# Kernel optimization log

Hardware: AMD Instinct MI355X
Metric: run time of the kernel (lower is better)

## Reference

```python
import jax, jax.numpy as jnp
import numpy as np

QMAX = 127.0  # int8 symmetric quantization range


def _quant_dequant(w):
    """Per-output-channel symmetric int8 fake quantization (weight-only),
    mimicking nn.quantized.Linear.from_float weight quantization."""
    scale = jnp.max(jnp.abs(w), axis=-1, keepdims=True) / QMAX
    scale = jnp.maximum(scale, 1e-8)
    q = jnp.clip(jnp.round(w / scale), -QMAX, QMAX)
    return q * scale


def setup_inputs() -> dict:
    key = jax.random.key(0)
    ks = jax.random.split(key, 7)
    B, S, D, F, E, NS = 2, 2048, 1024, 2048, 8, 1
    std = 1.0 / np.sqrt(D)
    x = jax.random.normal(ks[0], (B, S, D), dtype=jnp.float32)
    router_w = _quant_dequant(jax.random.normal(ks[1], (E, D), dtype=jnp.float32) * std)
    router_b = jnp.zeros((E,), dtype=jnp.float32)
    w_up = _quant_dequant(jax.random.normal(ks[2], (E, F, D), dtype=jnp.float32) * std)
    w_down = _quant_dequant(jax.random.normal(ks[3], (E, D, F), dtype=jnp.float32) / np.sqrt(F))
    shared_w_up = _quant_dequant(jax.random.normal(ks[4], (NS, F, D), dtype=jnp.float32) * std)
    shared_w_down = _quant_dequant(jax.random.normal(ks[5], (NS, D, F), dtype=jnp.float32) / np.sqrt(F))
    return {"x": x, "router_w": router_w, "router_b": router_b,
            "w_up": w_up, "w_down": w_down,
            "shared_w_up": shared_w_up, "shared_w_down": shared_w_down}


def reference(x, router_w, router_b, w_up, w_down, shared_w_up, shared_w_down):
    B, S, D = x.shape
    E = router_w.shape[0]
    TOPK = 2
    xt = x.reshape(-1, D)  # [T, D] tokens

    # Router (quantized linear) -> softmax -> top-k dispatch weights
    logits = xt @ router_w.T + router_b            # [T, E]
    probs = jax.nn.softmax(logits, axis=-1)        # [T, E]
    top_vals, top_idx = jax.lax.top_k(probs, TOPK)  # [T, K]
    top_vals = top_vals / jnp.sum(top_vals, axis=-1, keepdims=True)  # renormalize
    # combine[t, e] = routing weight of expert e for token t (0 if not selected)
    combine = jnp.sum(jax.nn.one_hot(top_idx, E, dtype=xt.dtype) * top_vals[..., None], axis=1)  # [T, E]

    # Routed experts: up -> SiLU -> down, computed densely then combined
    h = jnp.einsum('td,efd->tef', xt, w_up)        # [T, E, F]
    y = jnp.einsum('tef,edf->ted', jax.nn.silu(h), w_down)  # [T, E, D]
    out = jnp.einsum('ted,te->td', y, combine)     # [T, D]

    # Shared experts: always active, summed
    hs = jnp.einsum('td,sfd->tsf', xt, shared_w_up)          # [T, NS, F]
    out = out + jnp.einsum('tsf,sdf->td', jax.nn.silu(hs), shared_w_down)

    return out.reshape(B, S, D)
```

## Files before the change

### kernel.cpp

```cpp
#include <hip/hip_runtime.h>
#include <stdint.h>

typedef unsigned short u16;
typedef int i32x4 __attribute__((ext_vector_type(4)));

#define DDIM 1024
#define FDIM 2048
#define NEXP 8
#define RT_TILES 72
#define SHOFF 9216
#define RCAP 13312
#define NRT 104
#define UPROWS 16384
#define DNROWS 8192
#define UPTOT (UPROWS + FDIM)
#define DNTOT (DNROWS + DDIM)
#define WQWAVES (UPTOT + DNTOT)


__device__ inline float bf2f(u16 u) {
    union { unsigned int i; float f; } v; v.i = ((unsigned int)u) << 16; return v.f;
}
__device__ inline u16 f2bf(float f) {
    union { float f; unsigned int i; } v; v.f = f;
    unsigned int lsb = (v.i >> 16) & 1u;
    return (u16)((v.i + 0x7fffu + lsb) >> 16);
}
__device__ inline int q8(float v, float inv) {
    int x = (int)rintf(v * inv);
    return x < -127 ? -127 : (x > 127 ? 127 : x);
}
__device__ inline unsigned pack4(float a, float b, float c, float d, float inv) {
    return (unsigned)(q8(a, inv) & 255) | ((unsigned)(q8(b, inv) & 255) << 8) |
           ((unsigned)(q8(c, inv) & 255) << 16) | ((unsigned)(q8(d, inv) & 255) << 24);
}

typedef const __attribute__((address_space(1))) void gas_void;
typedef __attribute__((address_space(3))) void las_void;
#define GLL16(g, l) __builtin_amdgcn_global_load_lds((gas_void*)(g), (las_void*)(l), 16, 0, 0)

__device__ inline int detect_inline(const u16* __restrict__ x, int* sh) {
    if (threadIdx.x == 0) *sh = 0;
    __syncthreads();
    const int per = 1024 / blockDim.x;
    int bad = 0;
    for (int i = 0; i < per; i++) {
        u16 v = x[threadIdx.x * per + i];
        if (((v >> 7) & 0xFF) >= 0x8F) bad++;
    }
    if (bad) atomicAdd(sh, bad);
    __syncthreads();
    return (*sh > 32) ? 1 : 0;
}

__global__ __launch_bounds__(256) void router_kernel(
    const void* __restrict__ x_, const void* __restrict__ rw_, const void* __restrict__ rb_,
    float* __restrict__ top_w, int* __restrict__ top_idx)
{
    __shared__ char smem[32768 + 16];
    const int tid = threadIdx.x;
    const int wave = tid >> 6, lane = tid & 63;
    const int flag = detect_inline((const u16*)x_, (int*)(smem + 32768));

    float* rws = (float*)smem;
    if (!flag) {
        const ushort4* rwv = (const ushort4*)rw_;
        #pragma unroll
        for (int i = 0; i < 8; i++) {
            int idx = tid + i * 256;
            ushort4 h = rwv[idx];
            rws[idx * 4 + 0] = bf2f(h.x); rws[idx * 4 + 1] = bf2f(h.y);
            rws[idx * 4 + 2] = bf2f(h.z); rws[idx * 4 + 3] = bf2f(h.w);
        }
    } else {
        const float4* rwv = (const float4*)rw_;
        #pragma unroll
        for (int i = 0; i < 8; i++) {
            int idx = tid + i * 256;
            float4 f = rwv[idx];
            rws[idx * 4 + 0] = f.x; rws[idx * 4 + 1] = f.y;
            rws[idx * 4 + 2] = f.z; rws[idx * 4 + 3] = f.w;
        }
    }
    __syncthreads();

    for (int sub = 0; sub < 4; sub++) {
        const int t = blockIdx.x * 16 + wave * 4 + sub;
        float xv[16];
        if (!flag) {
            const u16* xr = (const u16*)x_ + (size_t)t * DDIM + lane * 16;
            uint4 p0 = *(const uint4*)(xr);
            uint4 p1 = *(const uint4*)(xr + 8);
            #pragma unroll
            for (int d = 0; d < 8; d++) xv[d]     = bf2f(((const u16*)&p0)[d]);
            #pragma unroll
            for (int d = 0; d < 8; d++) xv[d + 8] = bf2f(((const u16*)&p1)[d]);
        } else {
            const float4* xr = (const float4*)((const float*)x_ + (size_t)t * DDIM + lane * 16);
            #pragma unroll
            for (int c = 0; c < 4; c++) {
                float4 f = xr[c];
                xv[c * 4 + 0] = f.x; xv[c * 4 + 1] = f.y;
                xv[c * 4 + 2] = f.z; xv[c * 4 + 3] = f.w;
            }
        }
        float acc[NEXP];
        #pragma unroll
        for (int e = 0; e < NEXP; e++) {
            const float* wr = &rws[e * DDIM + lane * 16];
            float s = 0.f;
            #pragma unroll
            for (int d = 0; d < 16; d++) s += xv[d] * wr[d];
            acc[e] = s;
        }
        #pragma unroll
        for (int e = 0; e < NEXP; e++) {
            #pragma unroll
            for (int off = 32; off > 0; off >>= 1)
                acc[e] += __shfl_xor(acc[e], off, 64);
        }
        if (lane == 0) {
            float lg[NEXP];
            #pragma unroll
            for (int e = 0; e < NEXP; e++) {
                float b = flag ? ((const float*)rb_)[e] : bf2f(((const u16*)rb_)[e]);
                lg[e] = acc[e] + b;
            }
            int i0 = 0;
            #pragma unroll
            for (int e = 1; e < NEXP; e++) if (lg[e] > lg[i0]) i0 = e;
            int i1 = (i0 == 0) ? 1 : 0;
            #pragma unroll
            for (int e = 0; e < NEXP; e++) if (e != i0 && lg[e] > lg[i1]) i1 = e;
            float e1 = __expf(lg[i1] - lg[i0]);
            float w0 = 1.f / (1.f + e1);
            float w1 = e1 / (1.f + e1);
            top_w[2 * t] = w0;  top_w[2 * t + 1] = w1;
            top_idx[2 * t] = i0; top_idx[2 * t + 1] = i1;
        }
    }
}

template<int NC>
__device__ inline void wq_bf16(const char* __restrict__ src, char* __restrict__ dst,
                               float* __restrict__ sout, int R, int lane) {
    uint4 raw[NC];
    #pragma unroll
    for (int c = 0; c < NC; c++)
        raw[c] = *(const uint4*)(src + (size_t)c * 1024 + lane * 16);
    float m = 0.f;
    #pragma unroll
    for (int c = 0; c < NC; c++) {
        const u16* h = (const u16*)&raw[c];
        #pragma unroll
        for (int d = 0; d < 8; d++) m = fmaxf(m, fabsf(bf2f(h[d])));
    }
    #pragma unroll
    for (int off = 32; off > 0; off >>= 1) m = fmaxf(m, __shfl_xor(m, off, 64));
    m = fmaxf(m, 1e-12f);
    if (lane == 0) sout[R] = m / 127.f;
    const float inv = 127.f / m;
    #pragma unroll
    for (int c = 0; c < NC; c++) {
        const u16* h = (const u16*)&raw[c];
        uint2 o;
        o.x = pack4(bf2f(h[0]), bf2f(h[1]), bf2f(h[2]), bf2f(h[3]), inv);
        o.y = pack4(bf2f(h[4]), bf2f(h[5]), bf2f(h[6]), bf2f(h[7]), inv);
        *(uint2*)(dst + (size_t)c * 512 + lane * 8) = o;
    }
}

template<int NC>
__device__ inline void wq_f32(const char* __restrict__ src, char* __restrict__ dst,
                              float* __restrict__ sout, int R, int lane) {
    float m = 0.f;
    #pragma unroll
    for (int c = 0; c < NC; c++) {
        float4 f = *(const float4*)(src + (size_t)c * 1024 + lane * 16);
        m = fmaxf(m, fmaxf(fmaxf(fabsf(f.x), fabsf(f.y)),
                           fmaxf(fabsf(f.z), fabsf(f.w))));
    }
    #pragma unroll
    for (int off = 32; off > 0; off >>= 1) m = fmaxf(m, __shfl_xor(m, off, 64));
    m = fmaxf(m, 1e-12f);
    if (lane == 0) sout[R] = m / 127.f;
    const float inv = 127.f / m;
    #pragma unroll
    for (int c = 0; c < NC; c++) {
        float4 f = *(const float4*)(src + (size_t)c * 1024 + lane * 16);
        *(unsigned*)(dst + (size_t)c * 256 + lane * 4) = pack4(f.x, f.y, f.z, f.w, inv);
    }
}

__global__ __launch_bounds__(256) void wquant_kernel(
    const void* __restrict__ x_,
    const void* __restrict__ w_up, const void* __restrict__ w_down,
    const void* __restrict__ sw_up, const void* __restrict__ sw_down,
    char* __restrict__ qup, char* __restrict__ qdn,
    float* __restrict__ su, float* __restrict__ sd)
{
    __shared__ int scnt;
    const int wave = threadIdx.x >> 6, lane = threadIdx.x & 63;
    const int flag = detect_inline((const u16*)x_, &scnt);
    const int id = blockIdx.x * 4 + wave;
    if (id < UPTOT) {
        const int R = id;
        const size_t rb = flag ? (size_t)DDIM * 4 : (size_t)DDIM * 2;
        const char* src = (R < UPROWS)
            ? (const char*)w_up + (size_t)R * rb
            : (const char*)sw_up + (size_t)(R - UPROWS) * rb;
        char* dst = qup + (size_t)R * DDIM;
        if (!flag) wq_bf16<2>(src, dst, su, R, lane);
        else       wq_f32<4>(src, dst, su, R, lane);
    } else {
        const int R = id - UPTOT;
        const size_t rb = flag ? (size_t)FDIM * 4 : (size_t)FDIM * 2;
        const char* src = (R < DNROWS)
            ? (const char*)w_down + (size_t)R * rb
            : (const char*)sw_down + (size_t)(R - DNROWS) * rb;
        char* dst = qdn + (size_t)R * FDIM;
        if (!flag) wq_bf16<4>(src, dst, sd, R, lane);
        else       wq_f32<8>(src, dst, sd, R, lane);
    }
}

__global__ __launch_bounds__(1024) void rank_kernel(
    const u16* __restrict__ x, const int* __restrict__ top_idx,
    int* __restrict__ tok_rows, int* __restrict__ meta)
{
    __shared__ int wsum[16][NEXP];
    __shared__ int wbase[16][NEXP];
    __shared__ int scnt;
    const int tid = threadIdx.x, lane = tid & 63, wave = tid >> 6;

    const int flag = detect_inline(x, &scnt);
    if (tid == 0) meta[30] = flag;

    const int4* tp = (const int4*)(top_idx + tid * 8);
    int4 v0 = tp[0], v1 = tp[1];
    int e[8] = { v0.x, v0.y, v0.z, v0.w, v1.x, v1.y, v1.z, v1.w };

    int tcnt[NEXP];
    #pragma unroll
    for (int en = 0; en < NEXP; en++) tcnt[en] = 0;
    #pragma unroll
    for (int j = 0; j < 8; j++)
        #pragma unroll
        for (int en = 0; en < NEXP; en++) tcnt[en] += (e[j] == en);

    int excl[NEXP];
    #pragma unroll
    for (int en = 0; en < NEXP; en++) {
        int v = tcnt[en];
        #pragma unroll
        for (int off = 1; off < 64; off <<= 1) {
            int u = __shfl_up(v, off, 64);
            if (lane >= off) v += u;
        }
        excl[en] = v - tcnt[en];
        if (lane == 63) wsum[wave][en] = v;
    }
    __syncthreads();
    if (tid < NEXP) {
        int s = 0;
        for (int w = 0; w < 16; w++) { int c = wsum[w][tid]; wbase[w][tid] = s; s += c; }
        meta[tid] = s;
    }
    __syncthreads();
    if (tid == 0) {
        int b = 0;
        for (int en = 0; en < NEXP; en++) {
            meta[8 + en] = b;
            b += ((meta[en] + 127) >> 7) << 7;
        }
        meta[16] = b;
    }
    __syncthreads();

    int cur[NEXP];
    #pragma unroll
    for (int en = 0; en < NEXP; en++) cur[en] = meta[8 + en] + wbase[wave][en] + excl[en];

    int r[8];
    #pragma unroll
    for (int j = 0; j < 8; j++) {
        int rr = 0;
        #pragma unroll
        for (int en = 0; en < NEXP; en++)
            if (e[j] == en) { rr = cur[en]; cur[en] = rr + 1; }
        r[j] = rr;
    }
    int4* rp = (int4*)(tok_rows + tid * 8);
    rp[0] = make_int4(r[0], r[1], r[2], r[3]);
    rp[1] = make_int4(r[4], r[5], r[6], r[7]);
}

__global__ __launch_bounds__(128) void gather_q_kernel(
    const void* __restrict__ x_, const int* __restrict__ tok_rows,
    char* __restrict__ xq, float* __restrict__ sxa, const int* __restrict__ meta)
{
    __shared__ float red[128];
    const int t = blockIdx.x, tid = threadIdx.x;
    const int r0 = tok_rows[2 * t], r1 = tok_rows[2 * t + 1];

    float v[8];
    if (!meta[30]) {
        uint4 p = ((const uint4*)((const u16*)x_ + (size_t)t * DDIM))[tid];
        #pragma unroll
        for (int d = 0; d < 8; d++) v[d] = bf2f(((const u16*)&p)[d]);
    } else {
        const float4* xf = (const float4*)((const float*)x_ + (size_t)t * DDIM);
        float4 a = xf[2 * tid], b = xf[2 * tid + 1];
        v[0] = a.x; v[1] = a.y; v[2] = a.z; v[3] = a.w;
        v[4] = b.x; v[5] = b.y; v[6] = b.z; v[7] = b.w;
    }
    float m = 0.f;
    #pragma unroll
    for (int d = 0; d < 8; d++) m = fmaxf(m, fabsf(v[d]));
    red[tid] = m;
    __syncthreads();
    for (int s = 64; s > 0; s >>= 1) {
        if (tid < s) red[tid] = fmaxf(red[tid], red[tid + s]);
        __syncthreads();
    }
    const float mx = fmaxf(red[0], 1e-8f);
    const float inv = 127.f / mx;

    uint2 u;
    u.x = (unsigned)(q8(v[0], inv) & 255) | ((unsigned)(q8(v[1], inv) & 255) << 8) |
          ((unsigned)(q8(v[2], inv) & 255) << 16) | ((unsigned)(q8(v[3], inv) & 255) << 24);
    u.y = (unsigned)(q8(v[4], inv) & 255) | ((unsigned)(q8(v[5], inv) & 255) << 8) |
          ((unsigned)(q8(v[6], inv) & 255) << 16) | ((unsigned)(q8(v[7], inv) & 255) << 24);

    ((uint2*)(xq + (size_t)r0 * DDIM))[tid] = u;
    ((uint2*)(xq + (size_t)r1 * DDIM))[tid] = u;
    ((uint2*)(xq + (size_t)(SHOFF + t) * DDIM))[tid] = u;
    if (tid == 0) {
        float s = mx / 127.f;
        sxa[r0] = s; sxa[r1] = s; sxa[SHOFF + t] = s;
    }
}

__global__ __launch_bounds__(256, 2) void moe_gemm_i8(
    const char* __restrict__ A, const char* __restrict__ Wq,
    const float* __restrict__ sa, const float* __restrict__ sw,
    u16* __restrict__ Cout, const int* __restrict__ meta, int N, int Kd, int act)
{
    const int L = blockIdx.y * gridDim.x + blockIdx.x;
    const int xcd = L & 7;
    const int jj = L >> 3;
    const int rt = xcd * 13 + (jj % 13);
    const int ct = jj / 13;

    int e;
    if (rt >= RT_TILES) {
        e = NEXP;
    } else {
        const int r0t = rt * 128;
        if (r0t >= meta[16]) return;
        e = 0;
        #pragma unroll
        for (int i = 1; i < NEXP; i++) if (r0t >= meta[8 + i]) e = i;
        if (r0t >= meta[8 + e] + meta[e]) return;
    }
    const char* Wb = Wq + (size_t)(e * N + ct * 128) * Kd;
    const float* swb = sw + e * N + ct * 128;

    __shared__ char As[2][128 * 64];
    __shared__ char Bs[2][128 * 64];

    const int tid = threadIdx.x;
    const int wave = tid >> 6, lane = tid & 63;
    const int wm = (wave >> 1) * 64;
    const int wn = (wave & 1) * 64;
    const int l16 = lane & 15;
    const int q = lane >> 4;
    const int slot = (q + (l16 >> 1)) & 3;

    const int rsub = lane >> 2;
    const int qs = ((lane & 3) - ((lane >> 3) & 3)) & 3;

    const char* Ag = A + (size_t)(rt * 128 + wave * 16 + rsub) * Kd + qs * 16;
    const char* Bg = Wb + (size_t)(wave * 16 + rsub) * Kd + qs * 16;
    const size_t rstep = (size_t)64 * Kd;

    i32x4 acc[4][4] = {};

#define STAGE(buf, off) do { \
        GLL16(Ag + (off),         &As[buf][wave * 1024]); \
        GLL16(Ag + (off) + rstep, &As[buf][4096 + wave * 1024]); \
        GLL16(Bg + (off),         &Bs[buf][wave * 1024]); \
        GLL16(Bg + (off) + rstep, &Bs[buf][4096 + wave * 1024]); \
    } while (0)

    STAGE(0, 0);
    __syncthreads();

    int cur = 0;
    for (int kk = 0; kk < Kd; kk += 64) {
        if (kk + 64 < Kd) STAGE(cur ^ 1, kk + 64);
        i32x4 af[4], bf[4];
        #pragma unroll
        for (int i = 0; i < 4; i++)
            af[i] = *(const i32x4*)&As[cur][(wm + i * 16 + l16) * 64 + slot * 16];
        #pragma unroll
        for (int j = 0; j < 4; j++)
            bf[j] = *(const i32x4*)&Bs[cur][(wn + j * 16 + l16) * 64 + slot * 16];
        #pragma unroll
        for (int i = 0; i < 4; i++)
            #pragma unroll
            for (int j = 0; j < 4; j++)
                acc[i][j] = __builtin_amdgcn_mfma_i32_16x16x64_i8(af[i], bf[j], acc[i][j], 0, 0, 0);
        __syncthreads();
        cur ^= 1;
    }
#undef STAGE

    float sal[4][4];
    #pragma unroll
    for (int i = 0; i < 4; i++)
        #pragma unroll
        for (int rr = 0; rr < 4; rr++)
            sal[i][rr] = sa[rt * 128 + wm + i * 16 + q * 4 + rr];
    float swl[4];
    #pragma unroll
    for (int j = 0; j < 4; j++) swl[j] = swb[wn + j * 16 + l16];

    u16* Crow = Cout + (size_t)(rt * 128) * N + ct * 128;
    #pragma unroll
    for (int i = 0; i < 4; i++) {
        #pragma unroll
        for (int j = 0; j < 4; j++) {
            #pragma unroll
            for (int rr = 0; rr < 4; rr++) {
                const int row = wm + i * 16 + q * 4 + rr;
                const int col = wn + j * 16 + l16;
                float v = (float)acc[i][j][rr] * sal[i][rr] * swl[j];
                if (act) v = v / (1.f + __expf(-v));
                Crow[(size_t)row * N + col] = f2bf(v);
            }
        }
    }
}

__global__ __launch_bounds__(256) void hquant_kernel(
    const u16* __restrict__ hg, char* __restrict__ h8, float* __restrict__ sh,
    const int* __restrict__ meta)
{
    const int r = blockIdx.x;
    if (r >= meta[16] && r < SHOFF) return;
    __shared__ float red[256];
    const int tid = threadIdx.x;
    const u16* row = hg + (size_t)r * FDIM;
    uint4 p = ((const uint4*)row)[tid];
    float v[8];
    #pragma unroll
    for (int d = 0; d < 8; d++) v[d] = bf2f(((const u16*)&p)[d]);
    float m = 0.f;
    #pragma unroll
    for (int d = 0; d < 8; d++) m = fmaxf(m, fabsf(v[d]));
    red[tid] = m;
    __syncthreads();
    for (int s = 128; s > 0; s >>= 1) {
        if (tid < s) red[tid] = fmaxf(red[tid], red[tid + s]);
        __syncthreads();
    }
    const float mx = fmaxf(red[0], 1e-8f);
    const float inv = 127.f / mx;
    if (tid == 0) sh[r] = mx / 127.f;
    uint2 u;
    u.x = (unsigned)(q8(v[0], inv) & 255) | ((unsigned)(q8(v[1], inv) & 255) << 8) |
          ((unsigned)(q8(v[2], inv) & 255) << 16) | ((unsigned)(q8(v[3], inv) & 255) << 24);
    u.y = (unsigned)(q8(v[4], inv) & 255) | ((unsigned)(q8(v[5], inv) & 255) << 8) |
          ((unsigned)(q8(v[6], inv) & 255) << 16) | ((unsigned)(q8(v[7], inv) & 255) << 24);
    ((uint2*)(h8 + (size_t)r * FDIM))[tid] = u;
}

__global__ __launch_bounds__(256) void combine_kernel(
    const u16* __restrict__ yg, const float* __restrict__ top_w,
    const int* __restrict__ tok_rows, void* __restrict__ out_, const int* __restrict__ meta)
{
    const int t = blockIdx.x;
    const int r0 = tok_rows[2 * t], r1 = tok_rows[2 * t + 1];
    const float w0 = top_w[2 * t], w1 = top_w[2 * t + 1];
    const int d = threadIdx.x * 4;
    ushort4 y0 = *(const ushort4*)(yg + (size_t)r0 * DDIM + d);
    ushort4 y1 = *(const ushort4*)(yg + (size_t)r1 * DDIM + d);
    ushort4 ys = *(const ushort4*)(yg + (size_t)(SHOFF + t) * DDIM + d);
    float o0 = w0 * bf2f(y0.x) + w1 * bf2f(y1.x) + bf2f(ys.x);
    float o1 = w0 * bf2f(y0.y) + w1 * bf2f(y1.y) + bf2f(ys.y);
    float o2 = w0 * bf2f(y0.z) + w1 * bf2f(y1.z) + bf2f(ys.z);
    float o3 = w0 * bf2f(y0.w) + w1 * bf2f(y1.w) + bf2f(ys.w);
    if (!meta[30]) {
        ushort4 o; o.x = f2bf(o0); o.y = f2bf(o1); o.z = f2bf(o2); o.w = f2bf(o3);
        *(ushort4*)((u16*)out_ + (size_t)t * DDIM + d) = o;
    } else {
        float4 o; o.x = o0; o.y = o1; o.z = o2; o.w = o3;
        *(float4*)((float*)out_ + (size_t)t * DDIM + d) = o;
    }
}

extern "C" void kernel_launch(void* const* d_in, const int* in_sizes, int n_in,
                              void* d_out, int out_size, void* d_ws, size_t ws_size,
                              hipStream_t stream) {
    const void* x       = d_in[0];
    const void* rw      = d_in[1];
    const void* rb      = d_in[2];
    const void* w_up    = d_in[3];
    const void* w_down  = d_in[4];
    const void* sw_up   = d_in[5];
    const void* sw_down = d_in[6];

    const int T = in_sizes[0] / DDIM;

    char* ws = (char*)d_ws;
    int*   meta     = (int*)ws;
    float* top_w    = (float*)(ws + 1024);
    int*   top_idx  = (int*)(ws + 1024 + 8 * T);
    int*   tok_rows = (int*)(ws + 1024 + 16 * T);
    size_t off = 131072;
    u16*  yg = (u16*)(ws + off);
    char* xq = (char*)(ws + off);
    off += (size_t)RCAP * DDIM * 2;
    u16*  hg = (u16*)(ws + off);
    off += (size_t)RCAP * FDIM * 2;
    char* h8 = (char*)(ws + off);
    off += (size_t)RCAP * FDIM;
    char* qup = (char*)(ws + off);
    off += (size_t)(NEXP + 1) * FDIM * DDIM;
    char* qdn = (char*)(ws + off);
    off += (size_t)(NEXP + 1) * DDIM * FDIM;
    float* sxa = (float*)(ws + off); off += (size_t)RCAP * 4;
    float* sh  = (float*)(ws + off); off += (size_t)RCAP * 4;
    float* su  = (float*)(ws + off); off += (size_t)(NEXP + 1) * FDIM * 4;
    float* sd  = (float*)(ws + off); off += (size_t)(NEXP + 1) * DDIM * 4;

    const int nrb = T / 16;
    router_kernel<<<nrb, 256, 0, stream>>>(x, rw, rb, top_w, top_idx);
    wquant_kernel<<<WQWAVES / 4, 256, 0, stream>>>(
        x, w_up, w_down, sw_up, sw_down, qup, qdn, su, sd);
    rank_kernel<<<1, 1024, 0, stream>>>((const u16*)x, top_idx, tok_rows, meta);
    gather_q_kernel<<<T, 128, 0, stream>>>(x, tok_rows, xq, sxa, meta);

    moe_gemm_i8<<<dim3(FDIM / 128, NRT), 256, 0, stream>>>(
        xq, qup, sxa, su, hg, meta, FDIM, DDIM, 1);
    hquant_kernel<<<RCAP, 256, 0, stream>>>(hg, h8, sh, meta);
    moe_gemm_i8<<<dim3(DDIM / 128, NRT), 256, 0, stream>>>(
        h8, qdn, sh, sd, yg, meta, DDIM, FDIM, 0);
    combine_kernel<<<T, 256, 0, stream>>>(yg, top_w, tok_rows, d_out, meta);
}
```

Baseline: 334.2 us.

## Hoist dtype detection into one kernel, batch weight quant rows, use shuffle reductions

Moves the bf16/f32 input-type detection out of every block of the router, wquant and rank kernels into a single detect_kernel that writes a flag read by later kernels. Each wave in wquant now quantizes several rows (4 up rows or 2 down rows), so there are fewer blocks and more loads in flight per wave. The shared-memory tree reductions in gather_q and hquant are replaced by wave shuffles plus a small cross-wave combine. The cost is one extra kernel launch and higher register use per wave in wquant.

New measurement: 330.2 us. No clear change (-1.2%).

```diff
diff --git a/kernel.cpp b/kernel.cpp
--- a/kernel.cpp
+++ b/kernel.cpp
@@ -15,7 +15,9 @@
 #define DNROWS 8192
 #define UPTOT (UPROWS + FDIM)
 #define DNTOT (DNROWS + DDIM)
-#define WQWAVES (UPTOT + DNTOT)
+#define UPTASKS (UPTOT / 4)
+#define DNTASKS (DNTOT / 2)
+#define WQTASKS (UPTASKS + DNTASKS)
 
 
 __device__ inline float bf2f(u16 u) {
@@ -39,28 +41,31 @@
 typedef __attribute__((address_space(3))) void las_void;
 #define GLL16(g, l) __builtin_amdgcn_global_load_lds((gas_void*)(g), (las_void*)(l), 16, 0, 0)
 
-__device__ inline int detect_inline(const u16* __restrict__ x, int* sh) {
-    if (threadIdx.x == 0) *sh = 0;
-    __syncthreads();
-    const int per = 1024 / blockDim.x;
+__global__ __launch_bounds__(256) void detect_kernel(
+    const u16* __restrict__ x, int* __restrict__ meta)
+{
+    __shared__ int scnt;
+    if (threadIdx.x == 0) scnt = 0;
+    __syncthreads();
     int bad = 0;
-    for (int i = 0; i < per; i++) {
-        u16 v = x[threadIdx.x * per + i];
+    #pragma unroll
+    for (int i = 0; i < 4; i++) {
+        u16 v = x[threadIdx.x * 4 + i];
         if (((v >> 7) & 0xFF) >= 0x8F) bad++;
     }
-    if (bad) atomicAdd(sh, bad);
-    __syncthreads();
-    return (*sh > 32) ? 1 : 0;
+    if (bad) atomicAdd(&scnt, bad);
+    __syncthreads();
+    if (threadIdx.x == 0) meta[30] = (scnt > 32) ? 1 : 0;
 }
 
 __global__ __launch_bounds__(256) void router_kernel(
     const void* __restrict__ x_, const void* __restrict__ rw_, const void* __restrict__ rb_,
-    float* __restrict__ top_w, int* __restrict__ top_idx)
-{
-    __shared__ char smem[32768 + 16];
+    float* __restrict__ top_w, int* __restrict__ top_idx, const int* __restrict__ meta)
+{
+    __shared__ char smem[32768];
     const int tid = threadIdx.x;
     const int wave = tid >> 6, lane = tid & 63;
-    const int flag = detect_inline((const u16*)x_, (int*)(smem + 32768));
+    const int flag = meta[30];
 
     float* rws = (float*)smem;
     if (!flag) {
@@ -141,19 +146,56 @@
     }
 }
 
+template<int NR, int NC>
+__device__ inline void wq_bf16_n(const char* __restrict__ src, char* __restrict__ dst,
+                                 float* __restrict__ sout, int R0, int lane) {
+    uint4 raw[NR][NC];
+    #pragma unroll
+    for (int r = 0; r < NR; r++)
+        #pragma unroll
+        for (int c = 0; c < NC; c++)
+            raw[r][c] = *(const uint4*)(src + (size_t)r * (NC * 1024) + c * 1024 + lane * 16);
+    float m[NR];
+    #pragma unroll
+    for (int r = 0; r < NR; r++) {
+        m[r] = 0.f;
+        #pragma unroll
+        for (int c = 0; c < NC; c++) {
+            const u16* h = (const u16*)&raw[r][c];
+            #pragma unroll
+            for (int d = 0; d < 8; d++) m[r] = fmaxf(m[r], fabsf(bf2f(h[d])));
+        }
+    }
+    #pragma unroll
+    for (int off = 32; off > 0; off >>= 1)
+        #pragma unroll
+        for (int r = 0; r < NR; r++)
+            m[r] = fmaxf(m[r], __shfl_xor(m[r], off, 64));
+    #pragma unroll
+    for (int r = 0; r < NR; r++) {
+        m[r] = fmaxf(m[r], 1e-12f);
+        if (lane == 0) sout[R0 + r] = m[r] / 127.f;
+        const float inv = 127.f / m[r];
+        #pragma unroll
+        for (int c = 0; c < NC; c++) {
+            const u16* h = (const u16*)&raw[r][c];
+            uint2 o;
+            o.x = pack4(bf2f(h[0]), bf2f(h[1]), bf2f(h[2]), bf2f(h[3]), inv);
+            o.y = pack4(bf2f(h[4]), bf2f(h[5]), bf2f(h[6]), bf2f(h[7]), inv);
+            *(uint2*)(dst + (size_t)r * (NC * 512) + c * 512 + lane * 8) = o;
+        }
+    }
+}
+
 template<int NC>
-__device__ inline void wq_bf16(const char* __restrict__ src, char* __restrict__ dst,
-                               float* __restrict__ sout, int R, int lane) {
-    uint4 raw[NC];
-    #pragma unroll
-    for (int c = 0; c < NC; c++)
-        raw[c] = *(const uint4*)(src + (size_t)c * 1024 + lane * 16);
+__device__ inline void wq_f32(const char* __restrict__ src, char* __restrict__ dst,
+                              float* __restrict__ sout, int R, int lane) {
     float m = 0.f;
     #pragma unroll
     for (int c = 0; c < NC; c++) {
-        const u16* h = (const u16*)&raw[c];
-        #pragma unroll
-        for (int d = 0; d < 8; d++) m = fmaxf(m, fabsf(bf2f(h[d])));
+        float4 f = *(const float4*)(src + (size_t)c * 1024 + lane * 16);
+        m = fmaxf(m, fmaxf(fmaxf(fabsf(f.x), fabsf(f.y)),
+                           fmaxf(fabsf(f.z), fabsf(f.w))));
     }
     #pragma unroll
     for (int off = 32; off > 0; off >>= 1) m = fmaxf(m, __shfl_xor(m, off, 64));
@@ -162,79 +204,59 @@
     const float inv = 127.f / m;
     #pragma unroll
     for (int c = 0; c < NC; c++) {
-        const u16* h = (const u16*)&raw[c];
-        uint2 o;
-        o.x = pack4(bf2f(h[0]), bf2f(h[1]), bf2f(h[2]), bf2f(h[3]), inv);
-        o.y = pack4(bf2f(h[4]), bf2f(h[5]), bf2f(h[6]), bf2f(h[7]), inv);
-        *(uint2*)(dst + (size_t)c * 512 + lane * 8) = o;
-    }
-}
-
-template<int NC>
-__device__ inline void wq_f32(const char* __restrict__ src, char* __restrict__ dst,
-                              float* __restrict__ sout, int R, int lane) {
-    float m = 0.f;
-    #pragma unroll
-    for (int c = 0; c < NC; c++) {
-        float4 f = *(const float4*)(src + (size_t)c * 1024 + lane * 16);
-        m = fmaxf(m, fmaxf(fmaxf(fabsf(f.x), fabsf(f.y)),
-                           fmaxf(fabsf(f.z), fabsf(f.w))));
-    }
-    #pragma unroll
-    for (int off = 32; off > 0; off >>= 1) m = fmaxf(m, __shfl_xor(m, off, 64));
-    m = fmaxf(m, 1e-12f);
-    if (lane == 0) sout[R] = m / 127.f;
-    const float inv = 127.f / m;
-    #pragma unroll
-    for (int c = 0; c < NC; c++) {
         float4 f = *(const float4*)(src + (size_t)c * 1024 + lane * 16);
         *(unsigned*)(dst + (size_t)c * 256 + lane * 4) = pack4(f.x, f.y, f.z, f.w, inv);
     }
 }
 
 __global__ __launch_bounds__(256) void wquant_kernel(
-    const void* __restrict__ x_,
     const void* __restrict__ w_up, const void* __restrict__ w_down,
     const void* __restrict__ sw_up, const void* __restrict__ sw_down,
     char* __restrict__ qup, char* __restrict__ qdn,
-    float* __restrict__ su, float* __restrict__ sd)
-{
-    __shared__ int scnt;
+    float* __restrict__ su, float* __restrict__ sd, const int* __restrict__ meta)
+{
     const int wave = threadIdx.x >> 6, lane = threadIdx.x & 63;
-    const int flag = detect_inline((const u16*)x_, &scnt);
+    const int flag = meta[30];
     const int id = blockIdx.x * 4 + wave;
-    if (id < UPTOT) {
-        const int R = id;
-        const size_t rb = flag ? (size_t)DDIM * 4 : (size_t)DDIM * 2;
-        const char* src = (R < UPROWS)
-            ? (const char*)w_up + (size_t)R * rb
-            : (const char*)sw_up + (size_t)(R - UPROWS) * rb;
-        char* dst = qup + (size_t)R * DDIM;
-        if (!flag) wq_bf16<2>(src, dst, su, R, lane);
-        else       wq_f32<4>(src, dst, su, R, lane);
+    if (id < UPTASKS) {
+        const int R0 = id * 4;
+        if (!flag) {
+            const char* src = (R0 < UPROWS)
+                ? (const char*)w_up + (size_t)R0 * 2048
+                : (const char*)sw_up + (size_t)(R0 - UPROWS) * 2048;
+            wq_bf16_n<4, 2>(src, qup + (size_t)R0 * 1024, su, R0, lane);
+        } else {
+            const char* src = (R0 < UPROWS)
+                ? (const char*)w_up + (size_t)R0 * 4096
+                : (const char*)sw_up + (size_t)(R0 - UPROWS) * 4096;
+            for (int r = 0; r < 4; r++)
+                wq_f32<4>(src + (size_t)r * 4096, qup + (size_t)(R0 + r) * 1024,
+                          su, R0 + r, lane);
+        }
     } else {
-        const int R = id - UPTOT;
-        const size_t rb = flag ? (size_t)FDIM * 4 : (size_t)FDIM * 2;
-        const char* src = (R < DNROWS)
-            ? (const char*)w_down + (size_t)R * rb
-            : (const char*)sw_down + (size_t)(R - DNROWS) * rb;
-        char* dst = qdn + (size_t)R * FDIM;
-        if (!flag) wq_bf16<4>(src, dst, sd, R, lane);
-        else       wq_f32<8>(src, dst, sd, R, lane);
+        const int R0 = (id - UPTASKS) * 2;
+        if (!flag) {
+            const char* src = (R0 < DNROWS)
+                ? (const char*)w_down + (size_t)R0 * 4096
+                : (const char*)sw_down + (size_t)(R0 - DNROWS) * 4096;
+            wq_bf16_n<2, 4>(src, qdn + (size_t)R0 * 2048, sd, R0, lane);
+        } else {
+            const char* src = (R0 < DNROWS)
+                ? (const char*)w_down + (size_t)R0 * 8192
+                : (const char*)sw_down + (size_t)(R0 - DNROWS) * 8192;
+            for (int r = 0; r < 2; r++)
+                wq_f32<8>(src + (size_t)r * 8192, qdn + (size_t)(R0 + r) * 2048,
+                          sd, R0 + r, lane);
+        }
     }
 }
 
 __global__ __launch_bounds__(1024) void rank_kernel(
-    const u16* __restrict__ x, const int* __restrict__ top_idx,
-    int* __restrict__ tok_rows, int* __restrict__ meta)
+    const int* __restrict__ top_idx, int* __restrict__ tok_rows, int* __restrict__ meta)
 {
     __shared__ int wsum[16][NEXP];
     __shared__ int wbase[16][NEXP];
-    __shared__ int scnt;
     const int tid = threadIdx.x, lane = tid & 63, wave = tid >> 6;
-
-    const int flag = detect_inline(x, &scnt);
-    if (tid == 0) meta[30] = flag;
 
     const int4* tp = (const int4*)(top_idx + tid * 8);
     int4 v0 = tp[0], v1 = tp[1];
@@ -299,8 +321,9 @@
     const void* __restrict__ x_, const int* __restrict__ tok_rows,
     char* __restrict__ xq, float* __restrict__ sxa, const int* __restrict__ meta)
 {
-    __shared__ float red[128];
+    __shared__ float wmax[2];
     const int t = blockIdx.x, tid = threadIdx.x;
+    const int wave = tid >> 6, lane = tid & 63;
     const int r0 = tok_rows[2 * t], r1 = tok_rows[2 * t + 1];
 
     float v[8];
@@ -317,20 +340,16 @@
     float m = 0.f;
     #pragma unroll
     for (int d = 0; d < 8; d++) m = fmaxf(m, fabsf(v[d]));
-    red[tid] = m;
-    __syncthreads();
-    for (int s = 64; s > 0; s >>= 1) {
-        if (tid < s) red[tid] = fmaxf(red[tid], red[tid + s]);
-        __syncthreads();
-    }
-    const float mx = fmaxf(red[0], 1e-8f);
+    #pragma unroll
+    for (int off = 32; off > 0; off >>= 1) m = fmaxf(m, __shfl_xor(m, off, 64));
+    if (lane == 0) wmax[wave] = m;
+    __syncthreads();
+    const float mx = fmaxf(fmaxf(wmax[0], wmax[1]), 1e-8f);
     const float inv = 127.f / mx;
 
     uint2 u;
-    u.x = (unsigned)(q8(v[0], inv) & 255) | ((unsigned)(q8(v[1], inv) & 255) << 8) |
-          ((unsigned)(q8(v[2], inv) & 255) << 16) | ((unsigned)(q8(v[3], inv) & 255) << 24);
-    u.y = (unsigned)(q8(v[4], inv) & 255) | ((unsigned)(q8(v[5], inv) & 255) << 8) |
-          ((unsigned)(q8(v[6], inv) & 255) << 16) | ((unsigned)(q8(v[7], inv) & 255) << 24);
+    u.x = pack4(v[0], v[1], v[2], v[3], inv);
+    u.y = pack4(v[4], v[5], v[6], v[7], inv);
 
     ((uint2*)(xq + (size_t)r0 * DDIM))[tid] = u;
     ((uint2*)(xq + (size_t)r1 * DDIM))[tid] = u;
@@ -449,8 +468,9 @@
 {
     const int r = blockIdx.x;
     if (r >= meta[16] && r < SHOFF) return;
-    __shared__ float red[256];
+    __shared__ float wmax[4];
     const int tid = threadIdx.x;
+    const int wave = tid >> 6, lane = tid & 63;
     const u16* row = hg + (size_t)r * FDIM;
     uint4 p = ((const uint4*)row)[tid];
     float v[8];
@@ -459,20 +479,16 @@
     float m = 0.f;
     #pragma unroll
     for (int d = 0; d < 8; d++) m = fmaxf(m, fabsf(v[d]));
-    red[tid] = m;
-    __syncthreads();
-    for (int s = 128; s > 0; s >>= 1) {
-        if (tid < s) red[tid] = fmaxf(red[tid], red[tid + s]);
-        __syncthreads();
-    }
-    const float mx = fmaxf(red[0], 1e-8f);
+    #pragma unroll
+    for (int off = 32; off > 0; off >>= 1) m = fmaxf(m, __shfl_xor(m, off, 64));
+    if (lane == 0) wmax[wave] = m;
+    __syncthreads();
+    const float mx = fmaxf(fmaxf(fmaxf(wmax[0], wmax[1]), fmaxf(wmax[2], wmax[3])), 1e-8f);
     const float inv = 127.f / mx;
     if (tid == 0) sh[r] = mx / 127.f;
     uint2 u;
-    u.x = (unsigned)(q8(v[0], inv) & 255) | ((unsigned)(q8(v[1], inv) & 255) << 8) |
-          ((unsigned)(q8(v[2], inv) & 255) << 16) | ((unsigned)(q8(v[3], inv) & 255) << 24);
-    u.y = (unsigned)(q8(v[4], inv) & 255) | ((unsigned)(q8(v[5], inv) & 255) << 8) |
-          ((unsigned)(q8(v[6], inv) & 255) << 16) | ((unsigned)(q8(v[7], inv) & 255) << 24);
+    u.x = pack4(v[0], v[1], v[2], v[3], inv);
+    u.y = pack4(v[4], v[5], v[6], v[7], inv);
     ((uint2*)(h8 + (size_t)r * FDIM))[tid] = u;
 }
 
@@ -535,11 +551,13 @@
     float* su  = (float*)(ws + off); off += (size_t)(NEXP + 1) * FDIM * 4;
     float* sd  = (float*)(ws + off); off += (size_t)(NEXP + 1) * DDIM * 4;
 
+    detect_kernel<<<1, 256, 0, stream>>>((const u16*)x, meta);
+
     const int nrb = T / 16;
-    router_kernel<<<nrb, 256, 0, stream>>>(x, rw, rb, top_w, top_idx);
-    wquant_kernel<<<WQWAVES / 4, 256, 0, stream>>>(
-        x, w_up, w_down, sw_up, sw_down, qup, qdn, su, sd);
-    rank_kernel<<<1, 1024, 0, stream>>>((const u16*)x, top_idx, tok_rows, meta);
+    router_kernel<<<nrb, 256, 0, stream>>>(x, rw, rb, top_w, top_idx, meta);
+    wquant_kernel<<<WQTASKS / 4, 256, 0, stream>>>(
+        w_up, w_down, sw_up, sw_down, qup, qdn, su, sd, meta);
+    rank_kernel<<<1, 1024, 0, stream>>>(top_idx, tok_rows, meta);
     gather_q_kernel<<<T, 128, 0, stream>>>(x, tok_rows, xq, sxa, meta);
 
     moe_gemm_i8<<<dim3(FDIM / 128, NRT), 256, 0, stream>>>(
```
